# Performance work log

Measured on AMD Instinct MI355X. Metric: run time of the kernel, lower is better.

Reference implementation:

```python
import jax, jax.numpy as jnp
import numpy as np

C = 128  # in_dim = hidden_dim = out_dim = vector_dim
K = 16   # n_sample neighbors


def setup_inputs() -> dict:
    key = jax.random.key(0)
    ks = jax.random.split(key, 16)
    B, N = 4, 4096
    d = {}
    d["input_p"] = jax.random.normal(ks[0], (B, 3, N), jnp.float32)
    d["input_x"] = jax.random.normal(ks[1], (B, C, N), jnp.float32)

    def W(k_, o, i):
        return jax.random.normal(k_, (o, i), jnp.float32) * (1.0 / np.sqrt(i))

    # 1x1 conv weights (out,in) + biases
    specs = [("top", C), ("phi", C), ("psi", C), ("alpha", C), ("d1", 3),
             ("d2", C), ("g1", C), ("g2", C), ("down", C)]
    for j, (n, i) in enumerate(specs):
        d["W_" + n] = W(ks[2 + j], C, i)
        d["b_" + n] = jnp.zeros((C,), jnp.float32)
    # folded eval-mode BatchNorm: per-channel scale / shift
    for j, n in enumerate(["top", "d1", "d2", "g1", "g2", "down"]):
        kk = jax.random.fold_in(key, 100 + j)
        d["s_" + n] = 1.0 + 0.1 * jax.random.normal(kk, (C,), jnp.float32)
        d["t_" + n] = 0.1 * jax.random.normal(jax.random.fold_in(kk, 1), (C,), jnp.float32)
    return d


def _lin(x, Wm, b):
    # 1x1 conv == per-point linear; x: [..., in], Wm: [out, in]
    return jnp.einsum('oi,...i->...o', Wm, x) + b


def _bn(x, s, t):
    return x * s + t


def _forward(input_p, input_x,
             W_top, b_top, W_phi, b_phi, W_psi, b_psi, W_alpha, b_alpha,
             W_d1, b_d1, W_d2, b_d2, W_g1, b_g1, W_g2, b_g2, W_down, b_down,
             s_top, t_top, s_d1, t_d1, s_d2, t_d2, s_g1, t_g1, s_g2, t_g2,
             s_down, t_down):
    p = jnp.transpose(input_p, (0, 2, 1))   # [B,N,3]
    x = jnp.transpose(input_x, (0, 2, 1))   # [B,N,C]

    # ---- KNN: k nearest (squared euclidean, self included) ----
    sq = jnp.sum(p * p, -1)                                  # [B,N]
    d2 = sq[:, :, None] + sq[:, None, :] - 2.0 * jnp.einsum('bnd,bmd->bnm', p, p)
    _, idx = jax.lax.top_k(-d2, K)                           # [B,N,K]

    gather = jax.vmap(lambda f, i: f[i])                     # -> [B,N,K,feat]

    # ---- linear_top (conv1d + BN) ----
    top = _bn(_lin(x, W_top, b_top), s_top, t_top)           # [B,N,C]
    phi = _lin(top, W_phi, b_phi)                            # [B,N,C] (query)
    psi = _lin(top, W_psi, b_psi)                            # keys
    alp = _lin(top, W_alpha, b_alpha)                        # values

    psi_n = gather(psi, idx)                                 # [B,N,K,C]
    alp_n = gather(alp, idx)                                 # [B,N,K,C]
    p_n = gather(p, idx)                                     # [B,N,K,3]

    # ---- delta: positional encoding MLP on relative xyz ----
    rel = p[:, :, None, :] - p_n                             # [B,N,K,3]
    h = jax.nn.relu(_bn(_lin(rel, W_d1, b_d1), s_d1, t_d1))
    delta = _bn(_lin(h, W_d2, b_d2), s_d2, t_d2)             # [B,N,K,C]

    # ---- gamma: vector attention logits MLP ----
    g = phi[:, :, None, :] - psi_n + delta                   # [B,N,K,C]
    g = jax.nn.relu(_bn(_lin(g, W_g1, b_g1), s_g1, t_g1))
    g = _bn(_lin(g, W_g2, b_g2), s_g2, t_g2)                 # [B,N,K,C]

    attn = jax.nn.softmax(g, axis=2)                         # softmax over K neighbors
    y = jnp.sum(attn * (alp_n + delta), axis=2)              # [B,N,C]

    out = _bn(_lin(y, W_down, b_down), s_down, t_down) + x   # residual
    return jnp.transpose(out, (0, 2, 1))                     # [B,C,N]


def reference(input_p, input_x,
              W_top, b_top, W_phi, b_phi, W_psi, b_psi, W_alpha, b_alpha,
              W_d1, b_d1, W_d2, b_d2, W_g1, b_g1, W_g2, b_g2, W_down, b_down,
              s_top, t_top, s_d1, t_d1, s_d2, t_d2, s_g1, t_g1, s_g2, t_g2,
              s_down, t_down):
    return _forward(input_p, input_x,
                    W_top, b_top, W_phi, b_phi, W_psi, b_psi, W_alpha, b_alpha,
                    W_d1, b_d1, W_d2, b_d2, W_g1, b_g1, W_g2, b_g2,
                    W_down, b_down,
                    s_top, t_top, s_d1, t_d1, s_d2, t_d2, s_g1, t_g1,
                    s_g2, t_g2, s_down, t_down)
```

## Files before the change

kernel.cpp:

```cpp
#include <hip/hip_runtime.h>
#include <math.h>


#define NPTS 4096
#define BATCH 4
#define CDIM 128
#define KNBR 16
#define SA 68

__device__ __forceinline__ void load8(const float* __restrict__ v, int c0, float (&o)[8]) {
    float4 a = *(const float4*)&v[c0];
    float4 b = *(const float4*)&v[c0 + 4];
    o[0]=a.x; o[1]=a.y; o[2]=a.z; o[3]=a.w; o[4]=b.x; o[5]=b.y; o[6]=b.z; o[7]=b.w;
}

__device__ __forceinline__ void stage_wt_half(const float* __restrict__ gW, float* __restrict__ sW,
                                              int t, int k0) {
    const int kq = t & 15;
    const int cg = t >> 4;
    #pragma unroll
    for (int r = 0; r < 2; ++r) {
        const int c0 = (cg + r * 16) * 4;
        const int kk = kq * 4;
        float4 w0 = *(const float4*)&gW[(c0+0)*128 + k0 + kk];
        float4 w1 = *(const float4*)&gW[(c0+1)*128 + k0 + kk];
        float4 w2 = *(const float4*)&gW[(c0+2)*128 + k0 + kk];
        float4 w3 = *(const float4*)&gW[(c0+3)*128 + k0 + kk];
        const float r0v[4] = {w0.x,w0.y,w0.z,w0.w};
        const float r1v[4] = {w1.x,w1.y,w1.z,w1.w};
        const float r2v[4] = {w2.x,w2.y,w2.z,w2.w};
        const float r3v[4] = {w3.x,w3.y,w3.z,w3.w};
        #pragma unroll
        for (int j = 0; j < 4; ++j) {
            const int kl = kk + j;
            float4 v = make_float4(r0v[j], r1v[j], r2v[j], r3v[j]);
            *(float4*)&sW[kl*128 + (c0 ^ (kl & 0x7C))] = v;
        }
    }
}

__device__ __forceinline__ void gemm64(const float* __restrict__ sIn, const float* __restrict__ sW,
                                       int r0, int c0, float (&acc)[4][8]) {
    #pragma unroll 4
    for (int kl = 0; kl < 64; ++kl) {
        float4 a = *(const float4*)&sIn[kl*SA + r0];
        const int sw = kl & 0x7C;
        float4 b0 = *(const float4*)&sW[kl*128 + (c0 ^ sw)];
        float4 b1 = *(const float4*)&sW[kl*128 + ((c0+4) ^ sw)];
        const float av[4] = {a.x, a.y, a.z, a.w};
        const float bv[8] = {b0.x,b0.y,b0.z,b0.w,b1.x,b1.y,b1.z,b1.w};
        #pragma unroll
        for (int i = 0; i < 4; ++i)
            #pragma unroll
            for (int j = 0; j < 8; ++j)
                acc[i][j] = fmaf(av[i], bv[j], acc[i][j]);
    }
}

__device__ __forceinline__ void write_colmajor(float* __restrict__ sDst, int r0, int c0,
                                               const float (&v)[4][8]) {
    #pragma unroll
    for (int j = 0; j < 8; ++j) {
        float4 q = make_float4(v[0][j], v[1][j], v[2][j], v[3][j]);
        *(float4*)&sDst[(c0 + j)*SA + r0] = q;
    }
}

template<bool RELU>
__device__ __forceinline__ void epi_bn(float (&acc)[4][8], const float* __restrict__ bias,
                                       const float* __restrict__ sc, const float* __restrict__ sh, int c0) {
    float bb[8], ss[8], tt[8];
    load8(bias, c0, bb); load8(sc, c0, ss); load8(sh, c0, tt);
    #pragma unroll
    for (int i = 0; i < 4; ++i)
        #pragma unroll
        for (int j = 0; j < 8; ++j) {
            float v = fmaf(acc[i][j] + bb[j], ss[j], tt[j]);
            if (RELU) v = fmaxf(v, 0.f);
            acc[i][j] = v;
        }
}

__device__ __forceinline__ void epi_bias(float (&acc)[4][8], const float* __restrict__ bias, int c0) {
    float bb[8]; load8(bias, c0, bb);
    #pragma unroll
    for (int i = 0; i < 4; ++i)
        #pragma unroll
        for (int j = 0; j < 8; ++j) acc[i][j] += bb[j];
}

__device__ __forceinline__ void store_rows(float* __restrict__ dst, int b, int n0, int r0, int c0,
                                           const float (&v)[4][8]) {
    #pragma unroll
    for (int i = 0; i < 4; ++i) {
        float* row = &dst[((size_t)b*NPTS + n0 + r0 + i)*CDIM + c0];
        *(float4*)row     = make_float4(v[i][0], v[i][1], v[i][2], v[i][3]);
        *(float4*)(row+4) = make_float4(v[i][4], v[i][5], v[i][6], v[i][7]);
    }
}

__global__ __launch_bounds__(512)
void knn_kernel(const float* __restrict__ p, int* __restrict__ idx_out) {
    __shared__ float4 p4[NPTS];
    __shared__ float  mv[8*16*64];
    __shared__ int    mi[8*16*64];
    const int b = blockIdx.y, n0 = blockIdx.x*64, t = threadIdx.x;
    const float* pb = p + (size_t)b*3*NPTS;
    for (int m = t; m < NPTS; m += 512) {
        float xx = pb[m], yy = pb[NPTS+m], zz = pb[2*NPTS+m];
        p4[m] = make_float4(xx, yy, zz, xx*xx + yy*yy + zz*zz);
    }
    __syncthreads();
    const int w = t >> 6, l = t & 63;
    const float4 Q = p4[n0 + l];
    float bv[16]; int bi[16];
    #pragma unroll
    for (int j = 0; j < 16; ++j) { bv[j] = __builtin_inff(); bi[j] = 0x7FFFFFFF; }
    const int m0 = w * 512;
    for (int mm = 0; mm < 512; ++mm) {
        const int m = m0 + mm;
        const float4 P = p4[m];
        float dot = Q.x * P.x;
        dot = fmaf(Q.y, P.y, dot);
        dot = fmaf(Q.z, P.z, dot);
        const float d2 = fmaf(-2.f, dot, Q.w + P.w);
        if (d2 < bv[15]) {
            float cv = d2; int ci = m;
            #pragma unroll
            for (int j = 0; j < 16; ++j) {
                bool s_ = (cv < bv[j]);
                float tv = bv[j]; int ti = bi[j];
                bv[j] = s_ ? cv : tv;  bi[j] = s_ ? ci : ti;
                cv    = s_ ? tv : cv;  ci    = s_ ? ti : ci;
            }
        }
    }
    #pragma unroll
    for (int j = 0; j < 16; ++j) { mv[(w*16+j)*64 + l] = bv[j]; mi[(w*16+j)*64 + l] = bi[j]; }
    __syncthreads();
    if (t < 64) {
        const int q = t;
        float av[16]; int ai[16];
        #pragma unroll
        for (int j = 0; j < 16; ++j) { av[j] = mv[j*64+q]; ai[j] = mi[j*64+q]; }
        for (int w2 = 1; w2 < 8; ++w2) {
            float bw[16]; int bidx[16];
            #pragma unroll
            for (int j = 0; j < 16; ++j) { bw[j] = mv[(w2*16+j)*64+q]; bidx[j] = mi[(w2*16+j)*64+q]; }
            float cv[16]; int ci[16];
            #pragma unroll
            for (int j = 0; j < 16; ++j) {
                float a1 = av[j]; int a2 = ai[j];
                float b1 = bw[15-j]; int b2 = bidx[15-j];
                bool lt = (a1 < b1) || (a1 == b1 && a2 < b2);
                cv[j] = lt ? a1 : b1; ci[j] = lt ? a2 : b2;
            }
            #pragma unroll
            for (int gap = 8; gap >= 1; gap >>= 1) {
                #pragma unroll
                for (int i = 0; i < 16; ++i) {
                    if ((i & gap) == 0) {
                        const int k2 = i + gap;
                        bool le = (cv[i] < cv[k2]) || (cv[i] == cv[k2] && ci[i] < ci[k2]);
                        float tv = cv[i], tw = cv[k2]; int ti = ci[i], tj = ci[k2];
                        cv[i]  = le ? tv : tw; ci[i]  = le ? ti : tj;
                        cv[k2] = le ? tw : tv; ci[k2] = le ? tj : ti;
                    }
                }
            }
            #pragma unroll
            for (int j = 0; j < 16; ++j) { av[j] = cv[j]; ai[j] = ci[j]; }
        }
        int* orow = &idx_out[((size_t)b*NPTS + n0 + q)*KNBR];
        #pragma unroll
        for (int j = 0; j < 16; ++j) orow[j] = ai[j];
    }
}

__global__ __launch_bounds__(256, 2)
void top_proj_kernel(const float* __restrict__ x,
                     const float* __restrict__ Wt_, const float* __restrict__ bt_,
                     const float* __restrict__ st_, const float* __restrict__ tt_,
                     const float* __restrict__ Wph, const float* __restrict__ bph,
                     const float* __restrict__ Wps, const float* __restrict__ bps,
                     const float* __restrict__ Wal, const float* __restrict__ bal,
                     float* __restrict__ phi, float* __restrict__ psi, float* __restrict__ alp) {
    __shared__ float sX[128*SA];
    __shared__ float sW[64*128];
    const int t = threadIdx.x, tx = t & 15, ty = t >> 4;
    const int r0 = tx*4, c0 = ty*8;
    const int b = blockIdx.y, n0 = blockIdx.x*64;
    #pragma unroll
    for (int rr = 0; rr < 8; ++rr) {
        const int k = rr*16 + ty;
        *(float4*)&sX[k*SA + r0] = *(const float4*)&x[((size_t)b*CDIM + k)*NPTS + n0 + r0];
    }
    stage_wt_half(Wt_, sW, t, 0);
    __syncthreads();
    float topv[4][8] = {};
    gemm64(sX, sW, r0, c0, topv);
    __syncthreads();
    stage_wt_half(Wt_, sW, t, 64);
    __syncthreads();
    gemm64(sX + 64*SA, sW, r0, c0, topv);
    epi_bn<false>(topv, bt_, st_, tt_, c0);
    __syncthreads();
    write_colmajor(sX, r0, c0, topv);
    stage_wt_half(Wph, sW, t, 0);
    __syncthreads();
    {
        float a2[4][8] = {};
        gemm64(sX, sW, r0, c0, a2);
        __syncthreads(); stage_wt_half(Wph, sW, t, 64); __syncthreads();
        gemm64(sX + 64*SA, sW, r0, c0, a2);
        epi_bias(a2, bph, c0); store_rows(phi, b, n0, r0, c0, a2);
    }
    __syncthreads(); stage_wt_half(Wps, sW, t, 0); __syncthreads();
    {
        float a2[4][8] = {};
        gemm64(sX, sW, r0, c0, a2);
        __syncthreads(); stage_wt_half(Wps, sW, t, 64); __syncthreads();
        gemm64(sX + 64*SA, sW, r0, c0, a2);
        epi_bias(a2, bps, c0); store_rows(psi, b, n0, r0, c0, a2);
    }
    __syncthreads(); stage_wt_half(Wal, sW, t, 0); __syncthreads();
    {
        float a2[4][8] = {};
        gemm64(sX, sW, r0, c0, a2);
        __syncthreads(); stage_wt_half(Wal, sW, t, 64); __syncthreads();
        gemm64(sX + 64*SA, sW, r0, c0, a2);
        epi_bias(a2, bal, c0); store_rows(alp, b, n0, r0, c0, a2);
    }
}

__global__ __launch_bounds__(256, 2)
void pt_attn_kernel(const float* __restrict__ p,
                    const float* __restrict__ phi, const float* __restrict__ psi,
                    const float* __restrict__ alp, const int* __restrict__ idx,
                    const float* __restrict__ W_d1, const float* __restrict__ b_d1,
                    const float* __restrict__ W_d2, const float* __restrict__ b_d2,
                    const float* __restrict__ W_g1, const float* __restrict__ b_g1,
                    const float* __restrict__ W_g2, const float* __restrict__ b_g2,
                    const float* __restrict__ s_d1, const float* __restrict__ t_d1,
                    const float* __restrict__ s_d2, const float* __restrict__ t_d2,
                    const float* __restrict__ s_g1, const float* __restrict__ t_g1,
                    const float* __restrict__ s_g2, const float* __restrict__ t_g2,
                    float* __restrict__ yT) {
    __shared__ float sA[128*SA];
    __shared__ float sW[64*128];
    __shared__ float sWd1[3*128];
    __shared__ float sRel[3*SA];
    __shared__ float sPhi[4*132];
    __shared__ int   sIdx[64];
    const int t = threadIdx.x, tx = t & 15, ty = t >> 4;
    const int r0 = tx*4, c0 = ty*8;
    const int b = blockIdx.y, n0 = blockIdx.x*4;

    if (t < 64) sIdx[t] = idx[((size_t)b*NPTS + n0 + (t >> 4))*KNBR + (t & 15)];
    if (t < 128) {
        const int pt_ = t >> 5, cq = t & 31;
        *(float4*)&sPhi[pt_*132 + cq*4] = *(const float4*)&phi[((size_t)b*NPTS + n0 + pt_)*CDIM + cq*4];
    }
    if (t >= 128) {
        const int c = t - 128;
        #pragma unroll
        for (int j = 0; j < 3; ++j) sWd1[j*128 + c] = W_d1[c*3 + j];
    }
    stage_wt_half(W_d2, sW, t, 0);
    __syncthreads();
    if (t < 192) {
        const int j = t / 64, r = t % 64;
        const float pq = p[((size_t)b*3 + j)*NPTS + n0 + (r >> 4)];
        const float pn = p[((size_t)b*3 + j)*NPTS + sIdx[r]];
        sRel[j*SA + r] = pq - pn;
    }
    __syncthreads();
    {
        float acc[4][8] = {};
        #pragma unroll
        for (int k = 0; k < 3; ++k) {
            float4 a = *(const float4*)&sRel[k*SA + r0];
            float bv8[8]; load8(&sWd1[k*128], c0, bv8);
            const float av[4] = {a.x, a.y, a.z, a.w};
            #pragma unroll
            for (int i = 0; i < 4; ++i)
                #pragma unroll
                for (int j = 0; j < 8; ++j) acc[i][j] = fmaf(av[i], bv8[j], acc[i][j]);
        }
        epi_bn<true>(acc, b_d1, s_d1, t_d1, c0);
        write_colmajor(sA, r0, c0, acc);
    }
    __syncthreads();
    float dl[4][8] = {};
    gemm64(sA, sW, r0, c0, dl);
    __syncthreads();
    stage_wt_half(W_d2, sW, t, 64);
    __syncthreads();
    gemm64(sA + 64*SA, sW, r0, c0, dl);
    epi_bn<false>(dl, b_d2, s_d2, t_d2, c0);
    __syncthreads();
    {
        const int pt_ = tx >> 2;
        float ph[8]; load8(&sPhi[pt_*132], c0, ph);
        float g0[4][8];
        #pragma unroll
        for (int i = 0; i < 4; ++i) {
            const int jn = sIdx[r0 + i];
            float ps[8]; load8(&psi[((size_t)b*NPTS + jn)*CDIM], c0, ps);
            #pragma unroll
            for (int j = 0; j < 8; ++j) g0[i][j] = ph[j] - ps[j] + dl[i][j];
        }
        write_colmajor(sA, r0, c0, g0);
        stage_wt_half(W_g1, sW, t, 0);
    }
    __syncthreads();
    float g1[4][8] = {};
    gemm64(sA, sW, r0, c0, g1);
    __syncthreads();
    stage_wt_half(W_g1, sW, t, 64);
    __syncthreads();
    gemm64(sA + 64*SA, sW, r0, c0, g1);
    epi_bn<true>(g1, b_g1, s_g1, t_g1, c0);
    __syncthreads();
    write_colmajor(sA, r0, c0, g1);
    stage_wt_half(W_g2, sW, t, 0);
    __syncthreads();
    float g2[4][8] = {};
    gemm64(sA, sW, r0, c0, g2);
    __syncthreads();
    stage_wt_half(W_g2, sW, t, 64);
    __syncthreads();
    gemm64(sA + 64*SA, sW, r0, c0, g2);
    epi_bn<false>(g2, b_g2, s_g2, t_g2, c0);
    float den[8];
    #pragma unroll
    for (int j = 0; j < 8; ++j) {
        float m_ = fmaxf(fmaxf(g2[0][j], g2[1][j]), fmaxf(g2[2][j], g2[3][j]));
        m_ = fmaxf(m_, __shfl_xor(m_, 1));
        m_ = fmaxf(m_, __shfl_xor(m_, 2));
        float s_ = 0.f;
        #pragma unroll
        for (int i = 0; i < 4; ++i) { g2[i][j] = __expf(g2[i][j] - m_); s_ += g2[i][j]; }
        s_ += __shfl_xor(s_, 1);
        s_ += __shfl_xor(s_, 2);
        den[j] = s_;
    }
    float ya[8] = {};
    #pragma unroll
    for (int i = 0; i < 4; ++i) {
        const int jn = sIdx[r0 + i];
        float al[8]; load8(&alp[((size_t)b*NPTS + jn)*CDIM], c0, al);
        #pragma unroll
        for (int j = 0; j < 8; ++j) ya[j] = fmaf(g2[i][j], al[j] + dl[i][j], ya[j]);
    }
    #pragma unroll
    for (int j = 0; j < 8; ++j) {
        ya[j] += __shfl_xor(ya[j], 1);
        ya[j] += __shfl_xor(ya[j], 2);
    }
    if ((tx & 3) == 0) {
        const int pt_ = tx >> 2;
        #pragma unroll
        for (int j = 0; j < 8; ++j)
            yT[((size_t)b*CDIM + c0 + j)*NPTS + n0 + pt_] = ya[j] / den[j];
    }
}

__global__ __launch_bounds__(256, 2)
void down_kernel(const float* __restrict__ yT, const float* __restrict__ x,
                 const float* __restrict__ Wd, const float* __restrict__ bd,
                 const float* __restrict__ sd, const float* __restrict__ td,
                 float* __restrict__ out) {
    __shared__ float sY[128*SA];
    __shared__ float sW[64*128];
    const int t = threadIdx.x, tx = t & 15, ty = t >> 4;
    const int r0 = tx*4, c0 = ty*8;
    const int b = blockIdx.y, n0 = blockIdx.x*64;
    #pragma unroll
    for (int rr = 0; rr < 8; ++rr) {
        const int k = rr*16 + ty;
        *(float4*)&sY[k*SA + r0] = *(const float4*)&yT[((size_t)b*CDIM + k)*NPTS + n0 + r0];
    }
    stage_wt_half(Wd, sW, t, 0);
    __syncthreads();
    float acc[4][8] = {};
    gemm64(sY, sW, r0, c0, acc);
    __syncthreads();
    stage_wt_half(Wd, sW, t, 64);
    __syncthreads();
    gemm64(sY + 64*SA, sW, r0, c0, acc);
    epi_bn<false>(acc, bd, sd, td, c0);
    #pragma unroll
    for (int j = 0; j < 8; ++j) {
        const float* xrow = &x[((size_t)b*CDIM + c0 + j)*NPTS + n0 + r0];
        float4 res = *(const float4*)xrow;
        float4 o = make_float4(acc[0][j] + res.x, acc[1][j] + res.y,
                               acc[2][j] + res.z, acc[3][j] + res.w);
        *(float4*)&out[((size_t)b*CDIM + c0 + j)*NPTS + n0 + r0] = o;
    }
}

extern "C" void kernel_launch(void* const* d_in, const int* in_sizes, int n_in,
                              void* d_out, int out_size, void* d_ws, size_t ws_size,
                              hipStream_t stream) {
    const float* p    = (const float*)d_in[0];
    const float* x    = (const float*)d_in[1];
    const float* Wtop = (const float*)d_in[2];  const float* btop = (const float*)d_in[3];
    const float* Wphi = (const float*)d_in[4];  const float* bphi = (const float*)d_in[5];
    const float* Wpsi = (const float*)d_in[6];  const float* bpsi = (const float*)d_in[7];
    const float* Wal  = (const float*)d_in[8];  const float* bal  = (const float*)d_in[9];
    const float* Wd1  = (const float*)d_in[10]; const float* bd1  = (const float*)d_in[11];
    const float* Wd2  = (const float*)d_in[12]; const float* bd2  = (const float*)d_in[13];
    const float* Wg1  = (const float*)d_in[14]; const float* bg1  = (const float*)d_in[15];
    const float* Wg2  = (const float*)d_in[16]; const float* bg2  = (const float*)d_in[17];
    const float* Wdn  = (const float*)d_in[18]; const float* bdn  = (const float*)d_in[19];
    const float* stop = (const float*)d_in[20]; const float* ttop = (const float*)d_in[21];
    const float* sd1  = (const float*)d_in[22]; const float* td1  = (const float*)d_in[23];
    const float* sd2  = (const float*)d_in[24]; const float* td2  = (const float*)d_in[25];
    const float* sg1  = (const float*)d_in[26]; const float* tg1  = (const float*)d_in[27];
    const float* sg2  = (const float*)d_in[28]; const float* tg2  = (const float*)d_in[29];
    const float* sdn  = (const float*)d_in[30]; const float* tdn  = (const float*)d_in[31];

    char* ws = (char*)d_ws;
    int*   idx = (int*)ws;
    float* phi = (float*)(ws + (1 << 20));
    float* psi = phi + (size_t)BATCH*NPTS*CDIM;
    float* alp = psi + (size_t)BATCH*NPTS*CDIM;
    float* yT  = alp + (size_t)BATCH*NPTS*CDIM;

    dim3 gk(NPTS/64, BATCH);
    knn_kernel<<<gk, 512, 0, stream>>>(p, idx);
    dim3 g1(NPTS/64, BATCH);
    top_proj_kernel<<<g1, 256, 0, stream>>>(x, Wtop, btop, stop, ttop,
                                            Wphi, bphi, Wpsi, bpsi, Wal, bal,
                                            phi, psi, alp);
    dim3 g2(NPTS/4, BATCH);
    pt_attn_kernel<<<g2, 256, 0, stream>>>(p, phi, psi, alp, idx,
                                           Wd1, bd1, Wd2, bd2, Wg1, bg1, Wg2, bg2,
                                           sd1, td1, sd2, td2, sg1, tg1, sg2, tg2, yT);
    dim3 g3(NPTS/64, BATCH);
    down_kernel<<<g3, 256, 0, stream>>>(yT, x, Wdn, bdn, sdn, tdn, (float*)d_out);
}
```

Baseline: 1.006 ms.

## Precompute packed point coords globally and stream KNN candidates via scalar loads

Adds a small prep kernel that packs each point's xyz and squared norm into a float4 buffer in global memory. The KNN kernel drops its per-block 64KB shared-memory staging and instead reads candidates through a wave-uniform pointer, so the loads can go through the scalar cache. It also computes eight distances at a time before the insertion-sort step. This removes the redundant per-block staging and the shared-memory footprint, which may raise occupancy, at the cost of an extra kernel launch and a dependence on scalar-cache hits.

```diff
diff --git a/kernel.cpp b/kernel.cpp
--- a/kernel.cpp
+++ b/kernel.cpp
@@ -99,39 +99,47 @@
     }
 }
 
+__global__ __launch_bounds__(256)
+void prep_p4_kernel(const float* __restrict__ p, float4* __restrict__ p4g) {
+    const int b = blockIdx.y, n = blockIdx.x*256 + threadIdx.x;
+    const float* pb = p + (size_t)b*3*NPTS;
+    const float xx = pb[n], yy = pb[NPTS+n], zz = pb[2*NPTS+n];
+    p4g[(size_t)b*NPTS + n] = make_float4(xx, yy, zz, xx*xx + yy*yy + zz*zz);
+}
+
 __global__ __launch_bounds__(512)
-void knn_kernel(const float* __restrict__ p, int* __restrict__ idx_out) {
-    __shared__ float4 p4[NPTS];
+void knn_kernel(const float4* __restrict__ p4g, int* __restrict__ idx_out) {
     __shared__ float  mv[8*16*64];
     __shared__ int    mi[8*16*64];
     const int b = blockIdx.y, n0 = blockIdx.x*64, t = threadIdx.x;
-    const float* pb = p + (size_t)b*3*NPTS;
-    for (int m = t; m < NPTS; m += 512) {
-        float xx = pb[m], yy = pb[NPTS+m], zz = pb[2*NPTS+m];
-        p4[m] = make_float4(xx, yy, zz, xx*xx + yy*yy + zz*zz);
-    }
-    __syncthreads();
     const int w = t >> 6, l = t & 63;
-    const float4 Q = p4[n0 + l];
+    const float4 Q = p4g[(size_t)b*NPTS + n0 + l];
+    const int wu = __builtin_amdgcn_readfirstlane(w);
+    const float4* __restrict__ cand = p4g + (size_t)b*NPTS + wu*512;
     float bv[16]; int bi[16];
     #pragma unroll
     for (int j = 0; j < 16; ++j) { bv[j] = __builtin_inff(); bi[j] = 0x7FFFFFFF; }
-    const int m0 = w * 512;
-    for (int mm = 0; mm < 512; ++mm) {
-        const int m = m0 + mm;
-        const float4 P = p4[m];
-        float dot = Q.x * P.x;
-        dot = fmaf(Q.y, P.y, dot);
-        dot = fmaf(Q.z, P.z, dot);
-        const float d2 = fmaf(-2.f, dot, Q.w + P.w);
-        if (d2 < bv[15]) {
-            float cv = d2; int ci = m;
-            #pragma unroll
-            for (int j = 0; j < 16; ++j) {
-                bool s_ = (cv < bv[j]);
-                float tv = bv[j]; int ti = bi[j];
-                bv[j] = s_ ? cv : tv;  bi[j] = s_ ? ci : ti;
-                cv    = s_ ? tv : cv;  ci    = s_ ? ti : ci;
+    for (int mm = 0; mm < 512; mm += 8) {
+        float d[8];
+        #pragma unroll
+        for (int r = 0; r < 8; ++r) {
+            const float4 P = cand[mm + r];
+            float dot = Q.x * P.x;
+            dot = fmaf(Q.y, P.y, dot);
+            dot = fmaf(Q.z, P.z, dot);
+            d[r] = fmaf(-2.f, dot, Q.w + P.w);
+        }
+        #pragma unroll
+        for (int r = 0; r < 8; ++r) {
+            if (d[r] < bv[15]) {
+                float cv = d[r]; int ci = wu*512 + mm + r;
+                #pragma unroll
+                for (int j = 0; j < 16; ++j) {
+                    bool s_ = (cv < bv[j]);
+                    float tv = bv[j]; int ti = bi[j];
+                    bv[j] = s_ ? cv : tv;  bi[j] = s_ ? ci : ti;
+                    cv    = s_ ? tv : cv;  ci    = s_ ? ti : ci;
+                }
             }
         }
     }
@@ -427,9 +435,12 @@
     float* psi = phi + (size_t)BATCH*NPTS*CDIM;
     float* alp = psi + (size_t)BATCH*NPTS*CDIM;
     float* yT  = alp + (size_t)BATCH*NPTS*CDIM;
-
+    float4* p4g = (float4*)(yT + (size_t)BATCH*NPTS*CDIM);
+
+    dim3 gp(NPTS/256, BATCH);
+    prep_p4_kernel<<<gp, 256, 0, stream>>>(p, p4g);
     dim3 gk(NPTS/64, BATCH);
-    knn_kernel<<<gk, 512, 0, stream>>>(p, idx);
+    knn_kernel<<<gk, 512, 0, stream>>>(p4g, idx);
     dim3 g1(NPTS/64, BATCH);
     top_proj_kernel<<<g1, 256, 0, stream>>>(x, Wtop, btop, stop, ttop,
                                             Wphi, bphi, Wpsi, bpsi, Wal, bal,
```

New measurement: 1.045 ms. 3.9% more time.
